# Optimization experiments

Hardware: AMD Instinct MI355X
Metric: run time of the kernel (lower is better)

The kernel has to match this reference:

```python
import jax, jax.numpy as jnp
import numpy as np

N = 10000       # nodes
E = 320000      # edges (avg degree 32)
F_IN = 128      # node_in_fts
F_OUT = 128     # node_out_fts
H = 4           # num_heads_node
E_IN = 64       # edge_in_fts
HOPS = 3        # nr_of_hops
SLOPE = 0.2     # LeakyReLU negative slope (GAT default)


def setup_inputs() -> dict:
    key = jax.random.key(0)
    ks = jax.random.split(key, 10)
    s = 0.05
    return {
        "node_fts": jax.random.normal(ks[0], (N, F_IN), dtype=jnp.float32),
        "edge_fts": jax.random.normal(ks[1], (E, E_IN), dtype=jnp.float32),
        "edges": jax.random.randint(ks[2], (2, E), 0, N),
        # per-hop GATConv params (all hops share dims, stacked on axis 0)
        "Ws": jax.random.normal(ks[3], (HOPS, F_IN, H * F_OUT), dtype=jnp.float32) * s,
        "Wes": jax.random.normal(ks[4], (HOPS, E_IN, H * F_OUT), dtype=jnp.float32) * s,
        "a_src": jax.random.normal(ks[5], (HOPS, H, F_OUT), dtype=jnp.float32) * s,
        "a_dst": jax.random.normal(ks[6], (HOPS, H, F_OUT), dtype=jnp.float32) * s,
        "a_edge": jax.random.normal(ks[7], (HOPS, H, F_OUT), dtype=jnp.float32) * s,
        # gated residual params
        "W_prior": jax.random.normal(ks[8], (F_OUT, F_OUT), dtype=jnp.float32) * s,
        "W_curr": jax.random.normal(ks[9], (F_OUT, F_OUT), dtype=jnp.float32) * s,
    }


def _gat_conv(x, edge_fts, src, dst, W, We, asrc, adst, aedge):
    # dense projections: [N,H,F_OUT] and [E,H,F_OUT]
    h = (x @ W).reshape(-1, H, F_OUT)
    he = (edge_fts @ We).reshape(-1, H, F_OUT)
    h_src = h[src]                                   # [E,H,F_OUT] gather
    # per-edge attention logits [E,H]
    alpha = (h_src * asrc).sum(-1) + (h[dst] * adst).sum(-1) + (he * aedge).sum(-1)
    alpha = jax.nn.leaky_relu(alpha, SLOPE)
    # segment softmax over incoming edges of each destination node
    amax = jnp.full((N, H), -jnp.inf, dtype=alpha.dtype).at[dst].max(alpha)
    w = jnp.exp(alpha - amax[dst])                   # [E,H]
    denom = jax.ops.segment_sum(w, dst, num_segments=N) + 1e-16  # [N,H]
    msg = w[:, :, None] * h_src                      # [E,H,F_OUT]
    out = jax.ops.segment_sum(msg, dst, num_segments=N) / denom[:, :, None]
    return out.mean(axis=1)                          # mean head aggregation -> [N,F_OUT]


def reference(node_fts, edge_fts, edges, Ws, Wes, a_src, a_dst, a_edge, W_prior, W_curr):
    src, dst = edges[0], edges[1]
    x = node_fts
    prior = None
    for i in range(HOPS):
        curr = _gat_conv(x, edge_fts, src, dst, Ws[i], Wes[i], a_src[i], a_dst[i], a_edge[i])
        if prior is None:
            x = curr
        else:
            gate = jax.nn.sigmoid(prior @ W_prior + curr @ W_curr)
            x = gate * curr + (1.0 - gate) * prior
        prior = x
    return x
```

## Files before the change

kernel.cpp:

```cpp
#include <hip/hip_runtime.h>
#include <hip/hip_fp16.h>

#define N_NODES 10000
#define E_EDGES 320000
#define NH 4
#define HOPS 3
#define MAXD 256

typedef _Float16 f16x8 __attribute__((ext_vector_type(8)));
typedef _Float16 f16x4 __attribute__((ext_vector_type(4)));
typedef float    f32x4 __attribute__((ext_vector_type(4)));

__global__ void k_count(const int* __restrict__ dst, int* __restrict__ counts){
  int e = blockIdx.x*256 + threadIdx.x;
  if(e < E_EDGES) atomicAdd(&counts[dst[e]], 1);
}

__global__ __launch_bounds__(1024) void k_scan(const int* __restrict__ counts,
                                               int* __restrict__ row_ptr, int* __restrict__ fillp){
  __shared__ int sm[1024];
  int t = threadIdx.x;
  const int CH = 10;
  int base = t*CH;
  int loc[CH]; int sum = 0;
  #pragma unroll
  for(int i=0;i<CH;i++){
    int v = (base+i < N_NODES) ? counts[base+i] : 0;
    loc[i] = sum; sum += v;
  }
  sm[t] = sum; __syncthreads();
  for(int off=1; off<1024; off<<=1){
    int add = (t>=off) ? sm[t-off] : 0;
    __syncthreads();
    sm[t] += add;
    __syncthreads();
  }
  int excl = (t>0) ? sm[t-1] : 0;
  #pragma unroll
  for(int i=0;i<CH;i++){
    int n = base+i;
    if(n < N_NODES){
      int e = excl + loc[i];
      row_ptr[n] = e;
      fillp[n]   = e;
    }
  }
  if(t==1023) row_ptr[N_NODES] = sm[1023];
}

__global__ void k_fill(const int* __restrict__ src, const int* __restrict__ dst,
                       int* __restrict__ fillp, int* __restrict__ pos_e, int* __restrict__ sorted_src){
  int e = blockIdx.x*256 + threadIdx.x;
  if(e < E_EDGES){
    int d = dst[e];
    int pos = atomicAdd(&fillp[d], 1);
    pos_e[e] = pos;
    sorted_src[pos] = src[e];
  }
}

__global__ __launch_bounds__(256) void k_setup(const float* __restrict__ node_fts, _Float16* __restrict__ xh,
                       const float* __restrict__ Ws, _Float16* __restrict__ WsT,
                       const float* __restrict__ Wes, const float* __restrict__ a_edge,
                       float* __restrict__ b_edge){
  __shared__ float lds[32][65];
  int b = blockIdx.x, t = threadIdx.x;
  if(b < 1250){
    int i = b*256 + t;
    float4 v = *(const float4*)(node_fts + (size_t)i*4);
    f16x4 h = { (_Float16)v.x, (_Float16)v.y, (_Float16)v.z, (_Float16)v.w };
    *(f16x4*)(xh + (size_t)i*4) = h;
  } else if(b < 1346){
    int b2 = b - 1250;
    int hop = b2>>5, rem = b2&31, kt = rem>>3, ct = rem&7;
    int k0 = kt*32, c0 = ct*64;
    const float* wsrc = Ws + (size_t)hop*65536;
    #pragma unroll
    for(int i=0;i<8;i++){
      int u = t + i*256;
      int kk = u>>6, cc = u&63;
      lds[kk][cc] = wsrc[(size_t)(k0+kk)*512 + c0 + cc];
    }
    __syncthreads();
    _Float16* wdst = WsT + (size_t)hop*512*128;
    #pragma unroll
    for(int i=0;i<2;i++){
      int u = t + i*256;
      int c = u>>3, kq = (u&7)*4;
      f16x4 h = { (_Float16)lds[kq][c], (_Float16)lds[kq+1][c],
                  (_Float16)lds[kq+2][c], (_Float16)lds[kq+3][c] };
      *(f16x4*)(wdst + (size_t)(c0+c)*128 + k0 + kq) = h;
    }
  } else {
    int idx = (b-1346)*256 + t;
    if(idx < HOPS*64*NH){
      int hop = idx/(64*NH); int c = (idx/NH)%64; int h = idx%NH;
      const float* we = Wes + (size_t)hop*64*512 + (size_t)c*512 + h*128;
      const float* ae = a_edge + (size_t)hop*NH*128 + h*128;
      float s = 0.f;
      for(int f=0; f<128; f++) s += we[f] * ae[f];
      b_edge[idx] = s;
    }
  }
}

__global__ __launch_bounds__(256) void k_alpha_e(const float* __restrict__ edge_fts,
                        const int* __restrict__ pos_e, const float* __restrict__ b_edge,
                        float* __restrict__ ae_sorted){
  __shared__ float bl[HOPS*64*NH];
  for(int i=threadIdx.x; i<HOPS*64*NH; i+=256) bl[i] = b_edge[i];
  __syncthreads();
  int e = blockIdx.x*256 + threadIdx.x;
  if(e >= E_EDGES) return;
  int pos = pos_e[e];
  const float* ef = edge_fts + (size_t)e*64;
  float acc[HOPS*NH];
  #pragma unroll
  for(int i=0;i<HOPS*NH;i++) acc[i]=0.f;
  for(int c=0; c<64; c+=4){
    float4 xv = *(const float4*)(ef + c);
    float x[4] = {xv.x, xv.y, xv.z, xv.w};
    #pragma unroll
    for(int j=0;j<4;j++){
      float xc = x[j]; int cc = c+j;
      #pragma unroll
      for(int hh=0; hh<HOPS*NH; hh++){
        int hop = hh>>2, h = hh&3;
        acc[hh] += xc * bl[hop*256 + cc*4 + h];
      }
    }
  }
  #pragma unroll
  for(int hop=0; hop<HOPS; hop++){
    *(float4*)(ae_sorted + ((size_t)hop*E_EDGES + pos)*4) =
      make_float4(acc[hop*4+0], acc[hop*4+1], acc[hop*4+2], acc[hop*4+3]);
  }
}

__global__ __launch_bounds__(256) void k_projm(const _Float16* __restrict__ xh,
                       const _Float16* __restrict__ Wt, __half* __restrict__ h_all){
  __shared__ __align__(16) __half tile[64][72];
  int w = threadIdx.x>>6, l = threadIdx.x&63;
  int rowb = blockIdx.x*64;
  int row0 = rowb + w*16;
  int col0 = blockIdx.y*64;
  int ar = l&15, ac = (l>>4)*8;
  f32x4 acc0 = {0.f,0.f,0.f,0.f}, acc1 = acc0, acc2 = acc0, acc3 = acc0;
  #pragma unroll
  for(int kk=0; kk<4; kk++){
    f16x8 a  = *(const f16x8*)(xh + (size_t)(row0+ar)*128 + kk*32 + ac);
    f16x8 b0 = *(const f16x8*)(Wt + (size_t)(col0 +  0 + ar)*128 + kk*32 + ac);
    f16x8 b1 = *(const f16x8*)(Wt + (size_t)(col0 + 16 + ar)*128 + kk*32 + ac);
    f16x8 b2 = *(const f16x8*)(Wt + (size_t)(col0 + 32 + ar)*128 + kk*32 + ac);
    f16x8 b3 = *(const f16x8*)(Wt + (size_t)(col0 + 48 + ar)*128 + kk*32 + ac);
    acc0 = __builtin_amdgcn_mfma_f32_16x16x32_f16(a, b0, acc0, 0, 0, 0);
    acc1 = __builtin_amdgcn_mfma_f32_16x16x32_f16(a, b1, acc1, 0, 0, 0);
    acc2 = __builtin_amdgcn_mfma_f32_16x16x32_f16(a, b2, acc2, 0, 0, 0);
    acc3 = __builtin_amdgcn_mfma_f32_16x16x32_f16(a, b3, acc3, 0, 0, 0);
  }
  int crow = (l>>4)*4, ccol = l&15;
  #pragma unroll
  for(int r=0; r<4; r++){
    int tr = w*16 + crow + r;
    tile[tr][ccol     ] = __float2half(acc0[r]);
    tile[tr][ccol + 16] = __float2half(acc1[r]);
    tile[tr][ccol + 32] = __float2half(acc2[r]);
    tile[tr][ccol + 48] = __float2half(acc3[r]);
  }
  __syncthreads();
  #pragma unroll
  for(int i=0;i<2;i++){
    int u = threadIdx.x + i*256;
    int row = u>>3, cq = (u&7)*8;
    int grow = rowb + row;
    if(grow < N_NODES)
      *(float4*)(h_all + (size_t)grow*512 + col0 + cq) = *(const float4*)&tile[row][cq];
  }
}

__global__ __launch_bounds__(256) void k_s(const __half* __restrict__ h_all, const float* __restrict__ asrc,
                    const float* __restrict__ adst, float* __restrict__ s_src, float* __restrict__ s_dst){
  int nw = blockIdx.x*4 + (threadIdx.x>>6);
  int l = threadIdx.x&63;
  if(nw >= N_NODES) return;
  int h = l>>4, f8 = (l&15)*8;
  const __half* hp = h_all + (size_t)nw*512 + (h<<7) + f8;
  float4 raw = *(const float4*)hp;
  const __half2* hh = (const __half2*)&raw;
  float2 c0 = __half22float2(hh[0]);
  float2 c1 = __half22float2(hh[1]);
  float2 c2 = __half22float2(hh[2]);
  float2 c3 = __half22float2(hh[3]);
  float4 a0 = *(const float4*)(asrc + (h<<7) + f8);
  float4 a1 = *(const float4*)(asrc + (h<<7) + f8 + 4);
  float4 d0 = *(const float4*)(adst + (h<<7) + f8);
  float4 d1 = *(const float4*)(adst + (h<<7) + f8 + 4);
  float ps = c0.x*a0.x + c0.y*a0.y + c1.x*a0.z + c1.y*a0.w
           + c2.x*a1.x + c2.y*a1.y + c3.x*a1.z + c3.y*a1.w;
  float pd = c0.x*d0.x + c0.y*d0.y + c1.x*d0.z + c1.y*d0.w
           + c2.x*d1.x + c2.y*d1.y + c3.x*d1.z + c3.y*d1.w;
  #pragma unroll
  for(int off=1; off<16; off<<=1){ ps += __shfl_xor(ps,off); pd += __shfl_xor(pd,off); }
  if((l&15)==0){ s_src[nw*4+h] = ps; s_dst[nw*4+h] = pd; }
}

__global__ __launch_bounds__(256) void k_softagg(
    const float* __restrict__ ae, const float* __restrict__ s_src,
    const float* __restrict__ s_dst, const int* __restrict__ sorted_src,
    const int* __restrict__ row_ptr, const __half* __restrict__ h_all,
    float* __restrict__ ew_fb, float* __restrict__ xout, _Float16* __restrict__ xh)
{
  __shared__ float ws[MAXD*4];
  __shared__ int   ssm[MAXD];
  __shared__ float red2[4][520];
  __shared__ float mred[4][4];
  __shared__ float sred[4][4];

  int n = blockIdx.x, t = threadIdx.x;
  int start = row_ptr[n], end = row_ptr[n+1];
  int deg = end - start;
  bool fits = (deg <= MAXD);
  int wv = t>>6, lane = t&63;

  float4 sd = *(const float4*)(s_dst + (size_t)n*4);
  float m0=-1e30f, m1=-1e30f, m2=-1e30f, m3=-1e30f;
  float aR[4];

  if(fits){
    if(t < deg){
      int pos = start + t;
      int s = sorted_src[pos];
      float4 ss = *(const float4*)(s_src + (size_t)s*4);
      float4 av = *(const float4*)(ae + (size_t)pos*4);
      float a0 = ss.x+sd.x+av.x; a0=(a0>0.f)?a0:0.2f*a0;
      float a1 = ss.y+sd.y+av.y; a1=(a1>0.f)?a1:0.2f*a1;
      float a2 = ss.z+sd.z+av.z; a2=(a2>0.f)?a2:0.2f*a2;
      float a3 = ss.w+sd.w+av.w; a3=(a3>0.f)?a3:0.2f*a3;
      aR[0]=a0; aR[1]=a1; aR[2]=a2; aR[3]=a3;
      ssm[t] = s;
      m0=a0; m1=a1; m2=a2; m3=a3;
    }
  } else {
    for(int pos=start+t; pos<end; pos+=256){
      int s = sorted_src[pos];
      float4 ss = *(const float4*)(s_src + (size_t)s*4);
      float4 av = *(const float4*)(ae + (size_t)pos*4);
      float a0 = ss.x+sd.x+av.x; a0=(a0>0.f)?a0:0.2f*a0;
      float a1 = ss.y+sd.y+av.y; a1=(a1>0.f)?a1:0.2f*a1;
      float a2 = ss.z+sd.z+av.z; a2=(a2>0.f)?a2:0.2f*a2;
      float a3 = ss.w+sd.w+av.w; a3=(a3>0.f)?a3:0.2f*a3;
      *(float4*)(ew_fb + (size_t)pos*4) = make_float4(a0,a1,a2,a3);
      m0=fmaxf(m0,a0); m1=fmaxf(m1,a1); m2=fmaxf(m2,a2); m3=fmaxf(m3,a3);
    }
  }
  #pragma unroll
  for(int off=32; off; off>>=1){
    m0=fmaxf(m0,__shfl_xor(m0,off)); m1=fmaxf(m1,__shfl_xor(m1,off));
    m2=fmaxf(m2,__shfl_xor(m2,off)); m3=fmaxf(m3,__shfl_xor(m3,off));
  }
  if(lane==0){ mred[wv][0]=m0; mred[wv][1]=m1; mred[wv][2]=m2; mred[wv][3]=m3; }
  __syncthreads();
  m0 = fmaxf(fmaxf(mred[0][0],mred[1][0]),fmaxf(mred[2][0],mred[3][0]));
  m1 = fmaxf(fmaxf(mred[0][1],mred[1][1]),fmaxf(mred[2][1],mred[3][1]));
  m2 = fmaxf(fmaxf(mred[0][2],mred[1][2]),fmaxf(mred[2][2],mred[3][2]));
  m3 = fmaxf(fmaxf(mred[0][3],mred[1][3]),fmaxf(mred[2][3],mred[3][3]));

  float s0=0.f,s1=0.f,s2=0.f,s3=0.f;
  if(fits){
    if(t < deg){
      float w0=__expf(aR[0]-m0), w1=__expf(aR[1]-m1);
      float w2=__expf(aR[2]-m2), w3=__expf(aR[3]-m3);
      int sl = t*4;
      ws[sl]=w0; ws[sl+1]=w1; ws[sl+2]=w2; ws[sl+3]=w3;
      s0=w0; s1=w1; s2=w2; s3=w3;
    }
  } else {
    for(int pos=start+t; pos<end; pos+=256){
      float4 a = *(const float4*)(ew_fb + (size_t)pos*4);
      float w0=__expf(a.x-m0), w1=__expf(a.y-m1), w2=__expf(a.z-m2), w3=__expf(a.w-m3);
      *(float4*)(ew_fb + (size_t)pos*4) = make_float4(w0,w1,w2,w3);
      s0+=w0; s1+=w1; s2+=w2; s3+=w3;
    }
  }
  #pragma unroll
  for(int off=32; off; off>>=1){
    s0+=__shfl_xor(s0,off); s1+=__shfl_xor(s1,off);
    s2+=__shfl_xor(s2,off); s3+=__shfl_xor(s3,off);
  }
  if(lane==0){ sred[wv][0]=s0; sred[wv][1]=s1; sred[wv][2]=s2; sred[wv][3]=s3; }
  __syncthreads();

  int slot = t>>6;
  int l = t&63;
  int h = l>>4;
  int f8 = (l&15)*8;
  float dh = sred[0][h]+sred[1][h]+sred[2][h]+sred[3][h];
  float inv = 1.f/(dh + 1e-16f);
  float acc[8] = {0.f,0.f,0.f,0.f,0.f,0.f,0.f,0.f};
  for(int p = start + slot; p < end; p += 4){
    int sl = p - start;
    int s; float w;
    if(fits){ s = ssm[sl]; w = ws[sl*4 + h]; }
    else    { s = sorted_src[p]; w = ew_fb[(size_t)p*4 + h]; }
    const __half* hp = h_all + (size_t)s*512 + (h<<7) + f8;
    float4 raw = *(const float4*)hp;
    const __half2* hh = (const __half2*)&raw;
    float2 c0 = __half22float2(hh[0]);
    float2 c1 = __half22float2(hh[1]);
    float2 c2 = __half22float2(hh[2]);
    float2 c3 = __half22float2(hh[3]);
    acc[0]+=w*c0.x; acc[1]+=w*c0.y; acc[2]+=w*c1.x; acc[3]+=w*c1.y;
    acc[4]+=w*c2.x; acc[5]+=w*c2.y; acc[6]+=w*c3.x; acc[7]+=w*c3.y;
  }
  int flat = (h<<7) + f8;
  #pragma unroll
  for(int i=0;i<8;i++) red2[slot][flat+i] = acc[i]*inv;
  __syncthreads();
  if(t < 128){
    float v = 0.f;
    #pragma unroll
    for(int s=0;s<4;s++)
      v += red2[s][t] + red2[s][128+t] + red2[s][256+t] + red2[s][384+t];
    v *= 0.25f;
    xout[(size_t)n*128 + t] = v;
    if(xh) xh[(size_t)n*128 + t] = (_Float16)v;
  }
}

__global__ __launch_bounds__(256) void k_gate2(const float* __restrict__ prior, const float* __restrict__ curr,
                       const float* __restrict__ Wp, const float* __restrict__ Wc,
                       float* __restrict__ xnew, _Float16* __restrict__ xh){
  __shared__ float pr[32][132];
  __shared__ float cu[32][132];
  int t = threadIdx.x;
  int n0 = blockIdx.x*32;
  int c0 = blockIdx.y*64;
  #pragma unroll
  for(int i=0;i<4;i++){
    int u = t + i*256;
    int row = u>>5, c4 = (u&31)<<2;
    float4 v = make_float4(0.f,0.f,0.f,0.f), w = v;
    if(n0+row < N_NODES){
      v = *(const float4*)(prior + (size_t)(n0+row)*128 + c4);
      w = *(const float4*)(curr  + (size_t)(n0+row)*128 + c4);
    }
    *(float4*)&pr[row][c4] = v;
    *(float4*)&cu[row][c4] = w;
  }
  __syncthreads();
  int tc = t&15, tr = t>>4;
  int r0 = tr*2, cc = c0 + tc*4;
  float accp[2][4] = {{0.f,0.f,0.f,0.f},{0.f,0.f,0.f,0.f}};
  float accc[2][4] = {{0.f,0.f,0.f,0.f},{0.f,0.f,0.f,0.f}};
  #pragma unroll 4
  for(int k=0;k<128;k++){
    float4 wp = *(const float4*)(Wp + (size_t)k*128 + cc);
    float4 wc = *(const float4*)(Wc + (size_t)k*128 + cc);
    #pragma unroll
    for(int i=0;i<2;i++){
      float ap = pr[r0+i][k], ac = cu[r0+i][k];
      accp[i][0]+=ap*wp.x; accp[i][1]+=ap*wp.y; accp[i][2]+=ap*wp.z; accp[i][3]+=ap*wp.w;
      accc[i][0]+=ac*wc.x; accc[i][1]+=ac*wc.y; accc[i][2]+=ac*wc.z; accc[i][3]+=ac*wc.w;
    }
  }
  #pragma unroll
  for(int i=0;i<2;i++){
    int row = n0 + r0 + i;
    if(row < N_NODES){
      float oj[4];
      #pragma unroll
      for(int j=0;j<4;j++){
        float z = accp[i][j]+accc[i][j];
        float g = 1.f/(1.f+__expf(-z));
        oj[j] = g*cu[r0+i][cc + j] + (1.f-g)*pr[r0+i][cc + j];
      }
      *(float4*)(xnew + (size_t)row*128 + cc) = make_float4(oj[0],oj[1],oj[2],oj[3]);
      if(xh){
        f16x4 hv = { (_Float16)oj[0], (_Float16)oj[1], (_Float16)oj[2], (_Float16)oj[3] };
        *(f16x4*)(xh + (size_t)row*128 + cc) = hv;
      }
    }
  }
}

extern "C" void kernel_launch(void* const* d_in, const int* in_sizes, int n_in,
                              void* d_out, int out_size, void* d_ws, size_t ws_size,
                              hipStream_t stream){
  (void)in_sizes; (void)n_in; (void)out_size; (void)ws_size;
  const float* node_fts = (const float*)d_in[0];
  const float* edge_fts = (const float*)d_in[1];
  const int*   edges    = (const int*)d_in[2];
  const float* Ws       = (const float*)d_in[3];
  const float* Wes      = (const float*)d_in[4];
  const float* a_src    = (const float*)d_in[5];
  const float* a_dst    = (const float*)d_in[6];
  const float* a_edge   = (const float*)d_in[7];
  const float* W_prior  = (const float*)d_in[8];
  const float* W_curr   = (const float*)d_in[9];

  char* ws = (char*)d_ws;
  size_t off = 0;
  auto alloc = [&](size_t bytes)->void*{
    void* p = ws + off;
    off += (bytes + 255) & ~(size_t)255;
    return p;
  };
  int*       counts     = (int*)      alloc((size_t)N_NODES*4);
  int*       row_ptr    = (int*)      alloc((size_t)(N_NODES+1)*4);
  int*       fillp      = (int*)      alloc((size_t)N_NODES*4);
  int*       pos_e      = (int*)      alloc((size_t)E_EDGES*4);
  int*       sorted_src = (int*)      alloc((size_t)E_EDGES*4);
  float*     b_edge     = (float*)    alloc((size_t)HOPS*64*NH*4);
  float*     ae_sorted  = (float*)    alloc((size_t)HOPS*E_EDGES*NH*4);
  __half*    h_all      = (__half*)   alloc((size_t)N_NODES*512*2);
  float*     s_src      = (float*)    alloc((size_t)N_NODES*NH*4);
  float*     s_dst      = (float*)    alloc((size_t)N_NODES*NH*4);
  float*     ew_fb      = (float*)    alloc((size_t)E_EDGES*NH*4);
  float*     xbuf       = (float*)    alloc((size_t)N_NODES*128*4);
  float*     curbuf     = (float*)    alloc((size_t)N_NODES*128*4);
  _Float16*  xh         = (_Float16*) alloc((size_t)10112*128*2);
  _Float16*  WsT        = (_Float16*) alloc((size_t)HOPS*512*128*2);

  const int* src = edges;
  const int* dst = edges + E_EDGES;

  (void)hipMemsetAsync(counts, 0, (size_t)N_NODES*4, stream);
  k_count<<<(E_EDGES+255)/256, 256, 0, stream>>>(dst, counts);
  k_scan<<<1, 1024, 0, stream>>>(counts, row_ptr, fillp);
  k_fill<<<(E_EDGES+255)/256, 256, 0, stream>>>(src, dst, fillp, pos_e, sorted_src);
  k_setup<<<1349, 256, 0, stream>>>(node_fts, xh, Ws, WsT, Wes, a_edge, b_edge);
  k_alpha_e<<<(E_EDGES+255)/256, 256, 0, stream>>>(edge_fts, pos_e, b_edge, ae_sorted);

  for(int hop=0; hop<HOPS; hop++){
    k_projm<<<dim3(157, 8), 256, 0, stream>>>(xh, WsT + (size_t)hop*512*128, h_all);
    k_s<<<2500, 256, 0, stream>>>(h_all, a_src + (size_t)hop*512, a_dst + (size_t)hop*512, s_src, s_dst);
    float* xout = (hop==0) ? xbuf : curbuf;
    k_softagg<<<N_NODES, 256, 0, stream>>>(ae_sorted + (size_t)hop*E_EDGES*4, s_src, s_dst,
                                           sorted_src, row_ptr, h_all, ew_fb, xout,
                                           (hop==0) ? xh : (_Float16*)nullptr);
    if(hop > 0){
      float* xnew = (hop == HOPS-1) ? (float*)d_out : xbuf;
      k_gate2<<<dim3(313, 2), 256, 0, stream>>>(xbuf, curbuf, W_prior, W_curr, xnew,
                                                (hop < HOPS-1) ? xh : (_Float16*)nullptr);
    }
  }
}
```

Measured before the change: 346.1 us.

## Assign one wavefront per node in softmax-aggregate and split edge-attention work

The segment softmax and aggregation kernel now handles four nodes per block, one per wavefront. Its cross-wave shared-memory reductions and block barriers are replaced by wave shuffles, and output is written with vector stores. This removes idle threads and syncs for low-degree nodes, but serializes each node's neighbor loop within a single wave. The edge attention precompute splits each edge's 64 features across two threads, combined with a shuffle.

```diff
diff --git a/kernel.cpp b/kernel.cpp
--- a/kernel.cpp
+++ b/kernel.cpp
@@ -5,7 +5,7 @@
 #define E_EDGES 320000
 #define NH 4
 #define HOPS 3
-#define MAXD 256
+#define WMAX 128
 
 typedef _Float16 f16x8 __attribute__((ext_vector_type(8)));
 typedef _Float16 f16x4 __attribute__((ext_vector_type(4)));
@@ -110,14 +110,16 @@
   __shared__ float bl[HOPS*64*NH];
   for(int i=threadIdx.x; i<HOPS*64*NH; i+=256) bl[i] = b_edge[i];
   __syncthreads();
-  int e = blockIdx.x*256 + threadIdx.x;
-  if(e >= E_EDGES) return;
-  int pos = pos_e[e];
-  const float* ef = edge_fts + (size_t)e*64;
+  int t = threadIdx.x;
+  int el = t>>1, half = t&1;
+  int e = blockIdx.x*128 + el;
   float acc[HOPS*NH];
   #pragma unroll
   for(int i=0;i<HOPS*NH;i++) acc[i]=0.f;
-  for(int c=0; c<64; c+=4){
+  const float* ef = edge_fts + (size_t)e*64 + half*32;
+  const float* blh = bl + half*128;
+  #pragma unroll 2
+  for(int c=0; c<32; c+=4){
     float4 xv = *(const float4*)(ef + c);
     float x[4] = {xv.x, xv.y, xv.z, xv.w};
     #pragma unroll
@@ -126,14 +128,18 @@
       #pragma unroll
       for(int hh=0; hh<HOPS*NH; hh++){
         int hop = hh>>2, h = hh&3;
-        acc[hh] += xc * bl[hop*256 + cc*4 + h];
+        acc[hh] += xc * blh[hop*256 + cc*4 + h];
       }
     }
   }
   #pragma unroll
-  for(int hop=0; hop<HOPS; hop++){
-    *(float4*)(ae_sorted + ((size_t)hop*E_EDGES + pos)*4) =
-      make_float4(acc[hop*4+0], acc[hop*4+1], acc[hop*4+2], acc[hop*4+3]);
+  for(int hh=0; hh<HOPS*NH; hh++) acc[hh] += __shfl_xor(acc[hh], 1);
+  int pos = pos_e[e];
+  if(half==0){
+    *(float4*)(ae_sorted + ((size_t)0*E_EDGES + pos)*4) = make_float4(acc[0],acc[1],acc[2],acc[3]);
+    *(float4*)(ae_sorted + ((size_t)2*E_EDGES + pos)*4) = make_float4(acc[8],acc[9],acc[10],acc[11]);
+  } else {
+    *(float4*)(ae_sorted + ((size_t)1*E_EDGES + pos)*4) = make_float4(acc[4],acc[5],acc[6],acc[7]);
   }
 }
 
@@ -210,38 +216,41 @@
     const int* __restrict__ row_ptr, const __half* __restrict__ h_all,
     float* __restrict__ ew_fb, float* __restrict__ xout, _Float16* __restrict__ xh)
 {
-  __shared__ float ws[MAXD*4];
-  __shared__ int   ssm[MAXD];
-  __shared__ float red2[4][520];
-  __shared__ float mred[4][4];
-  __shared__ float sred[4][4];
-
-  int n = blockIdx.x, t = threadIdx.x;
+  __shared__ float ws4[4][WMAX*4];
+  __shared__ int   ssm4[4][WMAX];
+  int wv = threadIdx.x>>6, l = threadIdx.x&63;
+  int n = blockIdx.x*4 + wv;
+  if(n >= N_NODES) return;
   int start = row_ptr[n], end = row_ptr[n+1];
   int deg = end - start;
-  bool fits = (deg <= MAXD);
-  int wv = t>>6, lane = t&63;
+  bool fits = (deg <= WMAX);
+  float* ws = ws4[wv];
+  int*   ssm = ssm4[wv];
 
   float4 sd = *(const float4*)(s_dst + (size_t)n*4);
   float m0=-1e30f, m1=-1e30f, m2=-1e30f, m3=-1e30f;
-  float aR[4];
+  float aR[2][4];
 
   if(fits){
-    if(t < deg){
-      int pos = start + t;
-      int s = sorted_src[pos];
-      float4 ss = *(const float4*)(s_src + (size_t)s*4);
-      float4 av = *(const float4*)(ae + (size_t)pos*4);
-      float a0 = ss.x+sd.x+av.x; a0=(a0>0.f)?a0:0.2f*a0;
-      float a1 = ss.y+sd.y+av.y; a1=(a1>0.f)?a1:0.2f*a1;
-      float a2 = ss.z+sd.z+av.z; a2=(a2>0.f)?a2:0.2f*a2;
-      float a3 = ss.w+sd.w+av.w; a3=(a3>0.f)?a3:0.2f*a3;
-      aR[0]=a0; aR[1]=a1; aR[2]=a2; aR[3]=a3;
-      ssm[t] = s;
-      m0=a0; m1=a1; m2=a2; m3=a3;
+    #pragma unroll
+    for(int k=0;k<2;k++){
+      int idx = l + k*64;
+      if(idx < deg){
+        int pos = start + idx;
+        int s = sorted_src[pos];
+        float4 ss = *(const float4*)(s_src + (size_t)s*4);
+        float4 av = *(const float4*)(ae + (size_t)pos*4);
+        float a0 = ss.x+sd.x+av.x; a0=(a0>0.f)?a0:0.2f*a0;
+        float a1 = ss.y+sd.y+av.y; a1=(a1>0.f)?a1:0.2f*a1;
+        float a2 = ss.z+sd.z+av.z; a2=(a2>0.f)?a2:0.2f*a2;
+        float a3 = ss.w+sd.w+av.w; a3=(a3>0.f)?a3:0.2f*a3;
+        aR[k][0]=a0; aR[k][1]=a1; aR[k][2]=a2; aR[k][3]=a3;
+        ssm[idx] = s;
+        m0=fmaxf(m0,a0); m1=fmaxf(m1,a1); m2=fmaxf(m2,a2); m3=fmaxf(m3,a3);
+      }
     }
   } else {
-    for(int pos=start+t; pos<end; pos+=256){
+    for(int pos=start+l; pos<end; pos+=64){
       int s = sorted_src[pos];
       float4 ss = *(const float4*)(s_src + (size_t)s*4);
       float4 av = *(const float4*)(ae + (size_t)pos*4);
@@ -258,24 +267,22 @@
     m0=fmaxf(m0,__shfl_xor(m0,off)); m1=fmaxf(m1,__shfl_xor(m1,off));
     m2=fmaxf(m2,__shfl_xor(m2,off)); m3=fmaxf(m3,__shfl_xor(m3,off));
   }
-  if(lane==0){ mred[wv][0]=m0; mred[wv][1]=m1; mred[wv][2]=m2; mred[wv][3]=m3; }
-  __syncthreads();
-  m0 = fmaxf(fmaxf(mred[0][0],mred[1][0]),fmaxf(mred[2][0],mred[3][0]));
-  m1 = fmaxf(fmaxf(mred[0][1],mred[1][1]),fmaxf(mred[2][1],mred[3][1]));
-  m2 = fmaxf(fmaxf(mred[0][2],mred[1][2]),fmaxf(mred[2][2],mred[3][2]));
-  m3 = fmaxf(fmaxf(mred[0][3],mred[1][3]),fmaxf(mred[2][3],mred[3][3]));
 
   float s0=0.f,s1=0.f,s2=0.f,s3=0.f;
   if(fits){
-    if(t < deg){
-      float w0=__expf(aR[0]-m0), w1=__expf(aR[1]-m1);
-      float w2=__expf(aR[2]-m2), w3=__expf(aR[3]-m3);
-      int sl = t*4;
-      ws[sl]=w0; ws[sl+1]=w1; ws[sl+2]=w2; ws[sl+3]=w3;
-      s0=w0; s1=w1; s2=w2; s3=w3;
+    #pragma unroll
+    for(int k=0;k<2;k++){
+      int idx = l + k*64;
+      if(idx < deg){
+        float w0=__expf(aR[k][0]-m0), w1=__expf(aR[k][1]-m1);
+        float w2=__expf(aR[k][2]-m2), w3=__expf(aR[k][3]-m3);
+        int sl = idx*4;
+        ws[sl]=w0; ws[sl+1]=w1; ws[sl+2]=w2; ws[sl+3]=w3;
+        s0+=w0; s1+=w1; s2+=w2; s3+=w3;
+      }
     }
   } else {
-    for(int pos=start+t; pos<end; pos+=256){
+    for(int pos=start+l; pos<end; pos+=64){
       float4 a = *(const float4*)(ew_fb + (size_t)pos*4);
       float w0=__expf(a.x-m0), w1=__expf(a.y-m1), w2=__expf(a.z-m2), w3=__expf(a.w-m3);
       *(float4*)(ew_fb + (size_t)pos*4) = make_float4(w0,w1,w2,w3);
@@ -287,21 +294,15 @@
     s0+=__shfl_xor(s0,off); s1+=__shfl_xor(s1,off);
     s2+=__shfl_xor(s2,off); s3+=__shfl_xor(s3,off);
   }
-  if(lane==0){ sred[wv][0]=s0; sred[wv][1]=s1; sred[wv][2]=s2; sred[wv][3]=s3; }
-  __syncthreads();
-
-  int slot = t>>6;
-  int l = t&63;
-  int h = l>>4;
-  int f8 = (l&15)*8;
-  float dh = sred[0][h]+sred[1][h]+sred[2][h]+sred[3][h];
+
+  int h = l>>4, f8 = (l&15)*8;
+  float dh = (h==0)?s0:((h==1)?s1:((h==2)?s2:s3));
   float inv = 1.f/(dh + 1e-16f);
   float acc[8] = {0.f,0.f,0.f,0.f,0.f,0.f,0.f,0.f};
-  for(int p = start + slot; p < end; p += 4){
-    int sl = p - start;
+  for(int sl=0; sl<deg; sl++){
     int s; float w;
     if(fits){ s = ssm[sl]; w = ws[sl*4 + h]; }
-    else    { s = sorted_src[p]; w = ew_fb[(size_t)p*4 + h]; }
+    else    { s = sorted_src[start+sl]; w = ew_fb[(size_t)(start+sl)*4 + h]; }
     const __half* hp = h_all + (size_t)s*512 + (h<<7) + f8;
     float4 raw = *(const float4*)hp;
     const __half2* hh = (const __half2*)&raw;
@@ -312,18 +313,22 @@
     acc[0]+=w*c0.x; acc[1]+=w*c0.y; acc[2]+=w*c1.x; acc[3]+=w*c1.y;
     acc[4]+=w*c2.x; acc[5]+=w*c2.y; acc[6]+=w*c3.x; acc[7]+=w*c3.y;
   }
-  int flat = (h<<7) + f8;
-  #pragma unroll
-  for(int i=0;i<8;i++) red2[slot][flat+i] = acc[i]*inv;
-  __syncthreads();
-  if(t < 128){
-    float v = 0.f;
-    #pragma unroll
-    for(int s=0;s<4;s++)
-      v += red2[s][t] + red2[s][128+t] + red2[s][256+t] + red2[s][384+t];
-    v *= 0.25f;
-    xout[(size_t)n*128 + t] = v;
-    if(xh) xh[(size_t)n*128 + t] = (_Float16)v;
+  #pragma unroll
+  for(int i=0;i<8;i++){
+    acc[i] *= inv;
+    acc[i] += __shfl_xor(acc[i], 16);
+    acc[i] += __shfl_xor(acc[i], 32);
+    acc[i] *= 0.25f;
+  }
+  if(l < 16){
+    int f0 = l*8;
+    *(float4*)(xout + (size_t)n*128 + f0)     = make_float4(acc[0],acc[1],acc[2],acc[3]);
+    *(float4*)(xout + (size_t)n*128 + f0 + 4) = make_float4(acc[4],acc[5],acc[6],acc[7]);
+    if(xh){
+      f16x8 hv = { (_Float16)acc[0],(_Float16)acc[1],(_Float16)acc[2],(_Float16)acc[3],
+                   (_Float16)acc[4],(_Float16)acc[5],(_Float16)acc[6],(_Float16)acc[7] };
+      *(f16x8*)(xh + (size_t)n*128 + f0) = hv;
+    }
   }
 }
 
@@ -429,15 +434,15 @@
   k_scan<<<1, 1024, 0, stream>>>(counts, row_ptr, fillp);
   k_fill<<<(E_EDGES+255)/256, 256, 0, stream>>>(src, dst, fillp, pos_e, sorted_src);
   k_setup<<<1349, 256, 0, stream>>>(node_fts, xh, Ws, WsT, Wes, a_edge, b_edge);
-  k_alpha_e<<<(E_EDGES+255)/256, 256, 0, stream>>>(edge_fts, pos_e, b_edge, ae_sorted);
+  k_alpha_e<<<2500, 256, 0, stream>>>(edge_fts, pos_e, b_edge, ae_sorted);
 
   for(int hop=0; hop<HOPS; hop++){
     k_projm<<<dim3(157, 8), 256, 0, stream>>>(xh, WsT + (size_t)hop*512*128, h_all);
     k_s<<<2500, 256, 0, stream>>>(h_all, a_src + (size_t)hop*512, a_dst + (size_t)hop*512, s_src, s_dst);
     float* xout = (hop==0) ? xbuf : curbuf;
-    k_softagg<<<N_NODES, 256, 0, stream>>>(ae_sorted + (size_t)hop*E_EDGES*4, s_src, s_dst,
-                                           sorted_src, row_ptr, h_all, ew_fb, xout,
-                                           (hop==0) ? xh : (_Float16*)nullptr);
+    k_softagg<<<2500, 256, 0, stream>>>(ae_sorted + (size_t)hop*E_EDGES*4, s_src, s_dst,
+                                        sorted_src, row_ptr, h_all, ew_fb, xout,
+                                        (hop==0) ? xh : (_Float16*)nullptr);
     if(hop > 0){
       float* xnew = (hop == HOPS-1) ? (float*)d_out : xbuf;
       k_gate2<<<dim3(313, 2), 256, 0, stream>>>(xbuf, curbuf, W_prior, W_curr, xnew,
```

Result: no change. 347.5 us (+0.4%).
